# Kernel optimization log

Hardware: AMD Instinct MI355X
Metric: run time of the kernel (lower is better)

## Reference

```python
import jax, jax.numpy as jnp
import numpy as np

D_MODEL = 768
NUM_HEADS = 12
DEPTH = D_MODEL // NUM_HEADS


def setup_inputs() -> dict:
    key = jax.random.key(0)
    ks = jax.random.split(key, 11)
    B, S = 2, 2048
    scale = 1.0 / np.sqrt(D_MODEL)
    inp = {
        'v': jax.random.normal(ks[0], (B, S, D_MODEL), jnp.float32),
        'k': jax.random.normal(ks[1], (B, S, D_MODEL), jnp.float32),
        'q': jax.random.normal(ks[2], (B, S, D_MODEL), jnp.float32),
        'wq': jax.random.normal(ks[3], (D_MODEL, D_MODEL), jnp.float32) * scale,
        'bq': jnp.zeros((D_MODEL,), jnp.float32),
        'wk': jax.random.normal(ks[4], (D_MODEL, D_MODEL), jnp.float32) * scale,
        'bk': jnp.zeros((D_MODEL,), jnp.float32),
        'wv': jax.random.normal(ks[5], (D_MODEL, D_MODEL), jnp.float32) * scale,
        'bv': jnp.zeros((D_MODEL,), jnp.float32),
        'wo': jax.random.normal(ks[6], (D_MODEL, D_MODEL), jnp.float32) * scale,
        'bo': jnp.zeros((D_MODEL,), jnp.float32),
    }
    return inp


def _split_heads(x):
    B, S, _ = x.shape
    return x.reshape(B, S, NUM_HEADS, DEPTH).transpose(0, 2, 1, 3)  # [B,H,S,depth]


def reference(v, k, q, wq, bq, wk, bk, wv, bv, wo, bo):
    B, S, _ = q.shape
    qh = _split_heads(q @ wq + bq)  # [B,H,S,d]
    kh = _split_heads(k @ wk + bk)
    vh = _split_heads(v @ wv + bv)
    logits = jnp.einsum('bhqd,bhkd->bhqk', qh, kh) / jnp.sqrt(jnp.float32(DEPTH))
    attn = jax.nn.softmax(logits, axis=-1)  # [B,H,S,S]
    ctx = jnp.einsum('bhqk,bhkd->bhqd', attn, vh)
    concat = ctx.transpose(0, 2, 1, 3).reshape(B, S, D_MODEL)
    out = concat @ wo + bo
    return out, attn
```

## Files before the change

### kernel.cpp

```cpp
#include <hip/hip_runtime.h>

#define D_MODEL 768
#define NHEADS 12
#define DEPTH 64
#define SEQ 2048
#define NROWS 4096
#define KBLKS 24

typedef float f32x4 __attribute__((ext_vector_type(4)));
typedef short bf16x8 __attribute__((ext_vector_type(8)));
typedef unsigned u32x2 __attribute__((ext_vector_type(2)));
typedef unsigned u32x4 __attribute__((ext_vector_type(4)));

#define MFMA16(a, b, c) __builtin_amdgcn_mfma_f32_16x16x32_bf16((a), (b), (c), 0, 0, 0)

__device__ __forceinline__ short f2bf(float f) {
    union { float f; unsigned u; } v; v.f = f;
    unsigned r = (v.u + 0x7FFFu + ((v.u >> 16) & 1u)) >> 16;
    return (short)r;
}
__device__ __forceinline__ unsigned cvtpk(float a, float b) {
    unsigned r;
    asm("v_cvt_pk_bf16_f32 %0, %1, %2" : "=v"(r) : "v"(a), "v"(b));
    return r;
}

struct KF { bf16x8 a0, a1, b0, b1; };
struct VF { short4 x[8]; };

__device__ __forceinline__ KF loadK(const short* __restrict__ Kp, int k0, int r, int h) {
    KF f;
    const short* kr0 = Kp + (k0 + r) * DEPTH + 8 * h;
    const short* kr1 = kr0 + 16 * DEPTH;
    f.a0 = *(const bf16x8*)(kr0);
    f.a1 = *(const bf16x8*)(kr0 + 32);
    f.b0 = *(const bf16x8*)(kr1);
    f.b1 = *(const bf16x8*)(kr1 + 32);
    return f;
}
__device__ __forceinline__ VF loadV(const short* __restrict__ Vb, int k0, int r, int h) {
    VF f;
    const short* blk = Vb + (k0 >> 5) * (DEPTH * 32) + 4 * h;
#pragma unroll
    for (int nt = 0; nt < 4; nt++) {
        const short* row = blk + (16 * nt + r) * 32;
        f.x[2 * nt]     = *(const short4*)(row);
        f.x[2 * nt + 1] = *(const short4*)(row + 16);
    }
    return f;
}

__global__ __launch_bounds__(256) void xcast_kernel(
    const float* __restrict__ q, const float* __restrict__ k, const float* __restrict__ v,
    short* __restrict__ xb)
{
    int z = blockIdx.y;
    const float* src = (z == 0) ? q : (z == 1) ? k : v;
    int i = (blockIdx.x * 256 + threadIdx.x) * 8;
    int m = i / D_MODEL;
    int kk = i - m * D_MODEL;
    float4 f0 = *(const float4*)(src + i);
    float4 f1 = *(const float4*)(src + i + 4);
    u32x4 o;
    o[0] = cvtpk(f0.x, f0.y); o[1] = cvtpk(f0.z, f0.w);
    o[2] = cvtpk(f1.x, f1.y); o[3] = cvtpk(f1.z, f1.w);
    size_t off = ((size_t)(z * KBLKS + (kk >> 5)) * NROWS + m) * 32 + (kk & 31);
    *(u32x4*)(xb + off) = o;
}

__global__ __launch_bounds__(256) void wtrans_kernel(
    const float* __restrict__ wq, const float* __restrict__ wk,
    const float* __restrict__ wv, const float* __restrict__ wo,
    short* __restrict__ wt)
{
    __shared__ float tile[32][33];
    int wi = blockIdx.z;
    const float* W = (wi == 0) ? wq : (wi == 1) ? wk : (wi == 2) ? wv : wo;
    int k0 = blockIdx.x * 32, n0 = blockIdx.y * 32;
    int t = threadIdx.x;
    int tx = t & 31, ty = t >> 5;
#pragma unroll
    for (int i = 0; i < 4; i++) {
        int kk = ty + i * 8;
        tile[kk][tx] = W[(k0 + kk) * D_MODEL + n0 + tx];
    }
    __syncthreads();
    short* outb = wt + ((size_t)(wi * KBLKS + (k0 >> 5)) * D_MODEL) * 32;
#pragma unroll
    for (int i = 0; i < 4; i++) {
        int nn = ty + i * 8;
        outb[(size_t)(n0 + nn) * 32 + tx] = f2bf(tile[tx][nn]);
    }
}

__global__ __launch_bounds__(256) void qkv_gemm(
    const short* __restrict__ xb, const short* __restrict__ wt,
    const float* __restrict__ bq, const float* __restrict__ bk, const float* __restrict__ bv,
    short* __restrict__ qh, short* __restrict__ kh, short* __restrict__ vt)
{
    int z = blockIdx.z;
    int m0 = blockIdx.x * 64, n0 = blockIdx.y * 64;
    int lane = threadIdx.x & 63, w = threadIdx.x >> 6;
    int r = lane & 15, h = lane >> 4;

    const short* Ap = xb + ((size_t)z * KBLKS * NROWS + (m0 + 16 * w + r)) * 32 + 8 * h;
    const short* Bp = wt + ((size_t)z * KBLKS * D_MODEL) * 32;
    const int ASTEP = NROWS * 32, BSTEP = D_MODEL * 32;

    f32x4 acc[4] = {};
    bf16x8 ac = *(const bf16x8*)(Ap);
    bf16x8 bc[4];
#pragma unroll
    for (int nt = 0; nt < 4; nt++)
        bc[nt] = *(const bf16x8*)(Bp + (n0 + 16 * nt + r) * 32 + 8 * h);

    if (z == 2) {
        for (int kb = 0; kb < KBLKS; kb++) {
            int kn = (kb + 1 < KBLKS) ? kb + 1 : 0;
            bf16x8 an = *(const bf16x8*)(Ap + (size_t)kn * ASTEP);
            bf16x8 bn[4];
#pragma unroll
            for (int nt = 0; nt < 4; nt++)
                bn[nt] = *(const bf16x8*)(Bp + (size_t)kn * BSTEP + (n0 + 16 * nt + r) * 32 + 8 * h);
#pragma unroll
            for (int nt = 0; nt < 4; nt++)
                acc[nt] = MFMA16(ac, bc[nt], acc[nt]);
            ac = an;
#pragma unroll
            for (int nt = 0; nt < 4; nt++) bc[nt] = bn[nt];
        }
#pragma unroll
        for (int nt = 0; nt < 4; nt++) {
            int col = n0 + 16 * nt + r;
            float bsv = bv[col];
            int hh = col >> 6, dd = col & 63;
            int m = m0 + 16 * w + 4 * h;
            int b = m >> 11, s = m & 2047;
            short4 pk;
            pk.x = f2bf(acc[nt][0] + bsv);
            pk.y = f2bf(acc[nt][1] + bsv);
            pk.z = f2bf(acc[nt][2] + bsv);
            pk.w = f2bf(acc[nt][3] + bsv);
            long off = (((long)(b * NHEADS + hh) * 64 + (s >> 5)) * DEPTH + dd) * 32 + (s & 31);
            *(short4*)(vt + off) = pk;
        }
    } else {
        const float* bias = (z == 0) ? bq : bk;
        float scl = (z == 0) ? 0.18033688011112042f : 1.0f;
        short* dst = (z == 0) ? qh : kh;
        for (int kb = 0; kb < KBLKS; kb++) {
            int kn = (kb + 1 < KBLKS) ? kb + 1 : 0;
            bf16x8 an = *(const bf16x8*)(Ap + (size_t)kn * ASTEP);
            bf16x8 bn[4];
#pragma unroll
            for (int nt = 0; nt < 4; nt++)
                bn[nt] = *(const bf16x8*)(Bp + (size_t)kn * BSTEP + (n0 + 16 * nt + r) * 32 + 8 * h);
#pragma unroll
            for (int nt = 0; nt < 4; nt++)
                acc[nt] = MFMA16(bc[nt], ac, acc[nt]);
            ac = an;
#pragma unroll
            for (int nt = 0; nt < 4; nt++) bc[nt] = bn[nt];
        }
        int hh = n0 >> 6;
        int m = m0 + 16 * w + r;
        int b = m >> 11, s = m & 2047;
        long rowoff = ((long)(b * NHEADS + hh) * SEQ + s) * DEPTH;
#pragma unroll
        for (int nt = 0; nt < 4; nt++) {
            int dd = 16 * nt + 4 * h;
            float4 b4 = *(const float4*)(bias + n0 + dd);
            float v0 = (acc[nt][0] + b4.x) * scl;
            float v1 = (acc[nt][1] + b4.y) * scl;
            float v2 = (acc[nt][2] + b4.z) * scl;
            float v3 = (acc[nt][3] + b4.w) * scl;
            u32x2 pk = {cvtpk(v0, v1), cvtpk(v2, v3)};
            *(u32x2*)&dst[rowoff + dd] = pk;
        }
    }
}

__global__ __launch_bounds__(512, 4) void attn_kernel(
    const short* __restrict__ qh, const short* __restrict__ kh, const short* __restrict__ vt,
    float* __restrict__ attn, short* __restrict__ ctx)
{
    __shared__ float plds[64 * 256];
    __shared__ float sml[2][4][2][16];

    int wgid = blockIdx.x;
    int xcd = wgid & 7;
    int idx = wgid >> 3;
    int bh = xcd * 3 + (idx >> 5);
    int q0 = (idx & 31) * 64;

    int lane = threadIdx.x & 63, w = threadIdx.x >> 6;
    int wq2 = w >> 2, kc = w & 3;
    int r = lane & 15, h = lane >> 4;
    int qbase = q0 + 32 * wq2;

    const short* Qp = qh + ((long)bh * SEQ + qbase) * DEPTH;
    const short* Kp = kh + (long)bh * SEQ * DEPTH;
    const short* Vb = vt + (long)bh * (64 * DEPTH * 32);

    bf16x8 qf[2][2];
#pragma unroll
    for (int j = 0; j < 2; j++) {
        qf[j][0] = *(const bf16x8*)(Qp + (16 * j + r) * DEPTH + 8 * h);
        qf[j][1] = *(const bf16x8*)(Qp + (16 * j + r) * DEPTH + 32 + 8 * h);
    }

    float l0 = 0.f, l1 = 0.f;
    {
        int kstart = kc * 512, kend = kstart + 512;
        KF kcur = loadK(Kp, kstart, r, h);
        for (int k0 = kstart; k0 < kend; k0 += 32) {
            int kn = (k0 + 32 < kend) ? (k0 + 32) : kstart;
            KF knxt = loadK(Kp, kn, r, h);
#pragma unroll
            for (int j = 0; j < 2; j++) {
                f32x4 s0 = {}, s1 = {};
                s0 = MFMA16(kcur.a0, qf[j][0], s0);
                s1 = MFMA16(kcur.b0, qf[j][0], s1);
                s0 = MFMA16(kcur.a1, qf[j][1], s0);
                s1 = MFMA16(kcur.b1, qf[j][1], s1);
                float sum = exp2f(s0[0]) + exp2f(s0[1]) + exp2f(s0[2]) + exp2f(s0[3])
                          + exp2f(s1[0]) + exp2f(s1[1]) + exp2f(s1[2]) + exp2f(s1[3]);
                if (j == 0) l0 += sum; else l1 += sum;
            }
            kcur = knxt;
        }
    }
    l0 += __shfl_xor(l0, 16); l0 += __shfl_xor(l0, 32);
    l1 += __shfl_xor(l1, 16); l1 += __shfl_xor(l1, 32);
    if (lane < 16) {
        sml[wq2][kc][0][lane] = l0;
        sml[wq2][kc][1][lane] = l1;
    }
    __syncthreads();
    float rl[2];
#pragma unroll
    for (int j = 0; j < 2; j++)
        rl[j] = 1.0f / (sml[wq2][0][j][r] + sml[wq2][1][j][r] +
                        sml[wq2][2][j][r] + sml[wq2][3][j][r]);

    f32x4 o[2][4] = {};
    int rsw = r & 7;

    for (int chunk = 0; chunk < 8; chunk++) {
#pragma unroll
        for (int it = 0; it < 2; it++) {
            int k0 = chunk * 256 + kc * 64 + it * 32;
            KF kf = loadK(Kp, k0, r, h);
            VF vf = loadV(Vb, k0, r, h);
#pragma unroll
            for (int j = 0; j < 2; j++) {
                f32x4 s0 = {}, s1 = {};
                s0 = MFMA16(kf.a0, qf[j][0], s0);
                s1 = MFMA16(kf.b0, qf[j][0], s1);
                s0 = MFMA16(kf.a1, qf[j][1], s0);
                s1 = MFMA16(kf.b1, qf[j][1], s1);

                float p0 = exp2f(s0[0]) * rl[j], p1 = exp2f(s0[1]) * rl[j];
                float p2 = exp2f(s0[2]) * rl[j], p3 = exp2f(s0[3]) * rl[j];
                float p4 = exp2f(s1[0]) * rl[j], p5 = exp2f(s1[1]) * rl[j];
                float p6 = exp2f(s1[2]) * rl[j], p7 = exp2f(s1[3]) * rl[j];

                int row = wq2 * 32 + 16 * j + r;
                int G0 = kc * 16 + it * 8 + h;
                int G1 = G0 + 4;
                int pg0 = (G0 & ~7) | ((G0 & 7) ^ rsw);
                int pg1 = (G1 & ~7) | ((G1 & 7) ^ rsw);
                f32x4 v0 = {p0, p1, p2, p3};
                f32x4 v1 = {p4, p5, p6, p7};
                *(f32x4*)&plds[row * 256 + pg0 * 4] = v0;
                *(f32x4*)&plds[row * 256 + pg1 * 4] = v1;

                union { unsigned u[4]; bf16x8 v; } pa;
                pa.u[0] = cvtpk(p0, p1); pa.u[1] = cvtpk(p2, p3);
                pa.u[2] = cvtpk(p4, p5); pa.u[3] = cvtpk(p6, p7);
#pragma unroll
                for (int nt = 0; nt < 4; nt++) {
                    union { short4 s4[2]; bf16x8 v; } vv;
                    vv.s4[0] = vf.x[2 * nt];
                    vv.s4[1] = vf.x[2 * nt + 1];
                    o[j][nt] = MFMA16(vv.v, pa.v, o[j][nt]);
                }
            }
        }
        __syncthreads();

#pragma unroll
        for (int rr = 0; rr < 8; rr++) {
            int R = w * 8 + rr;
            float* arow = attn + ((long)(bh * SEQ + q0 + R)) * SEQ + chunk * 256;
            int pg = (lane & ~7) | ((lane & 7) ^ (R & 7));
            f32x4 val = *(const f32x4*)&plds[R * 256 + pg * 4];
            __builtin_nontemporal_store(val, (f32x4*)(arow + lane * 4));
        }
        __syncthreads();
    }

    if (kc != 0) {
#pragma unroll
        for (int j = 0; j < 2; j++)
#pragma unroll
            for (int nt = 0; nt < 4; nt++)
                *(f32x4*)&plds[((((wq2 * 3 + (kc - 1)) * 2 + j) * 4 + nt) * 64 + lane) * 4] =
                    o[j][nt];
    }
    __syncthreads();
    if (kc == 0) {
        int b = bh / NHEADS, head = bh % NHEADS;
#pragma unroll
        for (int j = 0; j < 2; j++) {
            long crow = ((long)(b * SEQ + qbase + 16 * j + r)) * D_MODEL + head * DEPTH;
#pragma unroll
            for (int nt = 0; nt < 4; nt++) {
                f32x4 acc = o[j][nt];
#pragma unroll
                for (int m = 0; m < 3; m++) {
                    f32x4 op = *(const f32x4*)
                        &plds[((((wq2 * 3 + m) * 2 + j) * 4 + nt) * 64 + lane) * 4];
                    acc[0] += op[0]; acc[1] += op[1];
                    acc[2] += op[2]; acc[3] += op[3];
                }
                *(unsigned*)&ctx[crow + 16 * nt + 4 * h]     = cvtpk(acc[0], acc[1]);
                *(unsigned*)&ctx[crow + 16 * nt + 4 * h + 2] = cvtpk(acc[2], acc[3]);
            }
        }
    }
}

__global__ __launch_bounds__(256) void out_gemm(
    const short* __restrict__ ctx, const short* __restrict__ wt,
    const float* __restrict__ bo, float* __restrict__ out)
{
    int m0 = blockIdx.x * 64, n0 = blockIdx.y * 64;
    int lane = threadIdx.x & 63, w = threadIdx.x >> 6;
    int r = lane & 15, h = lane >> 4;

    f32x4 acc[4] = {};
    const short* arow = ctx + (m0 + 16 * w + r) * D_MODEL;
    const short* Bp = wt + ((size_t)3 * KBLKS * D_MODEL) * 32;
    const int BSTEP = D_MODEL * 32;

    bf16x8 ac = *(const bf16x8*)(arow + 8 * h);
    bf16x8 bc[4];
#pragma unroll
    for (int nt = 0; nt < 4; nt++)
        bc[nt] = *(const bf16x8*)(Bp + (n0 + 16 * nt + r) * 32 + 8 * h);

    for (int kb = 0; kb < KBLKS; kb++) {
        int kn = (kb + 1 < KBLKS) ? kb + 1 : 0;
        bf16x8 an = *(const bf16x8*)(arow + kn * 32 + 8 * h);
        bf16x8 bn[4];
#pragma unroll
        for (int nt = 0; nt < 4; nt++)
            bn[nt] = *(const bf16x8*)(Bp + (size_t)kn * BSTEP + (n0 + 16 * nt + r) * 32 + 8 * h);
#pragma unroll
        for (int nt = 0; nt < 4; nt++)
            acc[nt] = MFMA16(bc[nt], ac, acc[nt]);
        ac = an;
#pragma unroll
        for (int nt = 0; nt < 4; nt++) bc[nt] = bn[nt];
    }
    int m = m0 + 16 * w + r;
#pragma unroll
    for (int nt = 0; nt < 4; nt++) {
        int n = n0 + 16 * nt + 4 * h;
        float4 b4 = *(const float4*)(bo + n);
        f32x4 res = {acc[nt][0] + b4.x, acc[nt][1] + b4.y,
                     acc[nt][2] + b4.z, acc[nt][3] + b4.w};
        *(f32x4*)(out + (long)m * D_MODEL + n) = res;
    }
}

extern "C" void kernel_launch(void* const* d_in, const int* in_sizes, int n_in,
                              void* d_out, int out_size, void* d_ws, size_t ws_size,
                              hipStream_t stream)
{
    const float* v  = (const float*)d_in[0];
    const float* k  = (const float*)d_in[1];
    const float* q  = (const float*)d_in[2];
    const float* wq = (const float*)d_in[3];
    const float* bq = (const float*)d_in[4];
    const float* wk = (const float*)d_in[5];
    const float* bk = (const float*)d_in[6];
    const float* wv = (const float*)d_in[7];
    const float* bv = (const float*)d_in[8];
    const float* wo = (const float*)d_in[9];
    const float* bo = (const float*)d_in[10];

    char* ws = (char*)d_ws;
    const size_t WT_BYTES  = (size_t)4 * D_MODEL * D_MODEL * 2;
    const size_t XB_BYTES  = (size_t)3 * NROWS * D_MODEL * 2;
    const size_t HB_BYTES  = (size_t)2 * NHEADS * SEQ * DEPTH * 2;
    short* wt  = (short*)(ws);
    short* xb  = (short*)(ws + WT_BYTES);
    short* qh  = (short*)(ws + WT_BYTES + XB_BYTES);
    short* kh  = (short*)(ws + WT_BYTES + XB_BYTES + HB_BYTES);
    short* vt  = (short*)(ws + WT_BYTES + XB_BYTES + 2 * HB_BYTES);
    short* ctx = (short*)(ws + WT_BYTES + XB_BYTES + 3 * HB_BYTES);

    float* out  = (float*)d_out;
    float* attn = (float*)d_out + (size_t)NROWS * D_MODEL;

    xcast_kernel<<<dim3(1536, 3), dim3(256), 0, stream>>>(q, k, v, xb);
    wtrans_kernel<<<dim3(24, 24, 4), dim3(256), 0, stream>>>(wq, wk, wv, wo, wt);
    qkv_gemm<<<dim3(64, 12, 3), dim3(256), 0, stream>>>(xb, wt, bq, bk, bv, qh, kh, vt);
    attn_kernel<<<dim3(768), dim3(512), 0, stream>>>(qh, kh, vt, attn, ctx);
    out_gemm<<<dim3(64, 12), dim3(256), 0, stream>>>(ctx, wt, bo, out);
}
```

Baseline: 267.5 us.

## Split softmax row-sum pass into a separate kernel writing reciprocal norms

Moves the first pass that computes softmax denominators out of attn_kernel into a new rl_kernel. It uses 384 blocks of 512 threads, each handling 128 queries with each wave covering half the key range, and writes reciprocal sums to a workspace buffer. attn_kernel then reads these values instead of recomputing them, which drops its LDS reduction and one barrier. The aim is to free attn_kernel's registers and schedule from the first pass and give the sum pass its own launch shape, at the cost of an extra launch and a small global round trip.

```diff
diff --git a/kernel.cpp b/kernel.cpp
--- a/kernel.cpp
+++ b/kernel.cpp
@@ -180,12 +180,72 @@
     }
 }
 
+__global__ __launch_bounds__(512) void rl_kernel(
+    const short* __restrict__ qh, const short* __restrict__ kh,
+    float* __restrict__ rlbuf)
+{
+    __shared__ float sml[4][2][2][16];
+
+    int wgid = blockIdx.x;
+    int xcd = wgid & 7;
+    int idx = wgid >> 3;
+    int bh = xcd * 3 + (idx >> 4);
+    int q0 = (idx & 15) * 128;
+
+    int lane = threadIdx.x & 63, w = threadIdx.x >> 6;
+    int wq2 = w >> 1, ksh = w & 1;
+    int r = lane & 15, h = lane >> 4;
+    int qbase = q0 + 32 * wq2;
+    int kstart = ksh * (SEQ / 2), kend = kstart + SEQ / 2;
+
+    const short* Qp = qh + ((long)bh * SEQ + qbase) * DEPTH;
+    const short* Kp = kh + (long)bh * SEQ * DEPTH;
+
+    bf16x8 qf[2][2];
+#pragma unroll
+    for (int j = 0; j < 2; j++) {
+        qf[j][0] = *(const bf16x8*)(Qp + (16 * j + r) * DEPTH + 8 * h);
+        qf[j][1] = *(const bf16x8*)(Qp + (16 * j + r) * DEPTH + 32 + 8 * h);
+    }
+
+    float l0 = 0.f, l1 = 0.f;
+    KF kcur = loadK(Kp, kstart, r, h);
+    for (int k0 = kstart; k0 < kend; k0 += 32) {
+        int kn = (k0 + 32 < kend) ? (k0 + 32) : kstart;
+        KF knxt = loadK(Kp, kn, r, h);
+#pragma unroll
+        for (int j = 0; j < 2; j++) {
+            f32x4 s0 = {}, s1 = {};
+            s0 = MFMA16(kcur.a0, qf[j][0], s0);
+            s1 = MFMA16(kcur.b0, qf[j][0], s1);
+            s0 = MFMA16(kcur.a1, qf[j][1], s0);
+            s1 = MFMA16(kcur.b1, qf[j][1], s1);
+            float sum = exp2f(s0[0]) + exp2f(s0[1]) + exp2f(s0[2]) + exp2f(s0[3])
+                      + exp2f(s1[0]) + exp2f(s1[1]) + exp2f(s1[2]) + exp2f(s1[3]);
+            if (j == 0) l0 += sum; else l1 += sum;
+        }
+        kcur = knxt;
+    }
+    l0 += __shfl_xor(l0, 16); l0 += __shfl_xor(l0, 32);
+    l1 += __shfl_xor(l1, 16); l1 += __shfl_xor(l1, 32);
+    if (lane < 16) {
+        sml[wq2][ksh][0][lane] = l0;
+        sml[wq2][ksh][1][lane] = l1;
+    }
+    __syncthreads();
+    if (ksh == 0 && lane < 16) {
+        float rl0 = 1.0f / (sml[wq2][0][0][lane] + sml[wq2][1][0][lane]);
+        float rl1 = 1.0f / (sml[wq2][0][1][lane] + sml[wq2][1][1][lane]);
+        rlbuf[bh * SEQ + qbase + lane]      = rl0;
+        rlbuf[bh * SEQ + qbase + 16 + lane] = rl1;
+    }
+}
+
 __global__ __launch_bounds__(512, 4) void attn_kernel(
     const short* __restrict__ qh, const short* __restrict__ kh, const short* __restrict__ vt,
-    float* __restrict__ attn, short* __restrict__ ctx)
+    const float* __restrict__ rlbuf, float* __restrict__ attn, short* __restrict__ ctx)
 {
     __shared__ float plds[64 * 256];
-    __shared__ float sml[2][4][2][16];
 
     int wgid = blockIdx.x;
     int xcd = wgid & 7;
@@ -208,40 +268,10 @@
         qf[j][0] = *(const bf16x8*)(Qp + (16 * j + r) * DEPTH + 8 * h);
         qf[j][1] = *(const bf16x8*)(Qp + (16 * j + r) * DEPTH + 32 + 8 * h);
     }
-
-    float l0 = 0.f, l1 = 0.f;
-    {
-        int kstart = kc * 512, kend = kstart + 512;
-        KF kcur = loadK(Kp, kstart, r, h);
-        for (int k0 = kstart; k0 < kend; k0 += 32) {
-            int kn = (k0 + 32 < kend) ? (k0 + 32) : kstart;
-            KF knxt = loadK(Kp, kn, r, h);
-#pragma unroll
-            for (int j = 0; j < 2; j++) {
-                f32x4 s0 = {}, s1 = {};
-                s0 = MFMA16(kcur.a0, qf[j][0], s0);
-                s1 = MFMA16(kcur.b0, qf[j][0], s1);
-                s0 = MFMA16(kcur.a1, qf[j][1], s0);
-                s1 = MFMA16(kcur.b1, qf[j][1], s1);
-                float sum = exp2f(s0[0]) + exp2f(s0[1]) + exp2f(s0[2]) + exp2f(s0[3])
-                          + exp2f(s1[0]) + exp2f(s1[1]) + exp2f(s1[2]) + exp2f(s1[3]);
-                if (j == 0) l0 += sum; else l1 += sum;
-            }
-            kcur = knxt;
-        }
-    }
-    l0 += __shfl_xor(l0, 16); l0 += __shfl_xor(l0, 32);
-    l1 += __shfl_xor(l1, 16); l1 += __shfl_xor(l1, 32);
-    if (lane < 16) {
-        sml[wq2][kc][0][lane] = l0;
-        sml[wq2][kc][1][lane] = l1;
-    }
-    __syncthreads();
     float rl[2];
 #pragma unroll
     for (int j = 0; j < 2; j++)
-        rl[j] = 1.0f / (sml[wq2][0][j][r] + sml[wq2][1][j][r] +
-                        sml[wq2][2][j][r] + sml[wq2][3][j][r]);
+        rl[j] = rlbuf[bh * SEQ + qbase + 16 * j + r];
 
     f32x4 o[2][4] = {};
     int rsw = r & 7;
@@ -395,12 +425,14 @@
     const size_t WT_BYTES  = (size_t)4 * D_MODEL * D_MODEL * 2;
     const size_t XB_BYTES  = (size_t)3 * NROWS * D_MODEL * 2;
     const size_t HB_BYTES  = (size_t)2 * NHEADS * SEQ * DEPTH * 2;
+    const size_t CTX_BYTES = (size_t)NROWS * D_MODEL * 2;
     short* wt  = (short*)(ws);
     short* xb  = (short*)(ws + WT_BYTES);
     short* qh  = (short*)(ws + WT_BYTES + XB_BYTES);
     short* kh  = (short*)(ws + WT_BYTES + XB_BYTES + HB_BYTES);
     short* vt  = (short*)(ws + WT_BYTES + XB_BYTES + 2 * HB_BYTES);
     short* ctx = (short*)(ws + WT_BYTES + XB_BYTES + 3 * HB_BYTES);
+    float* rlb = (float*)(ws + WT_BYTES + XB_BYTES + 3 * HB_BYTES + CTX_BYTES);
 
     float* out  = (float*)d_out;
     float* attn = (float*)d_out + (size_t)NROWS * D_MODEL;
@@ -408,6 +440,7 @@
     xcast_kernel<<<dim3(1536, 3), dim3(256), 0, stream>>>(q, k, v, xb);
     wtrans_kernel<<<dim3(24, 24, 4), dim3(256), 0, stream>>>(wq, wk, wv, wo, wt);
     qkv_gemm<<<dim3(64, 12, 3), dim3(256), 0, stream>>>(xb, wt, bq, bk, bv, qh, kh, vt);
-    attn_kernel<<<dim3(768), dim3(512), 0, stream>>>(qh, kh, vt, attn, ctx);
+    rl_kernel<<<dim3(384), dim3(512), 0, stream>>>(qh, kh, rlb);
+    attn_kernel<<<dim3(768), dim3(512), 0, stream>>>(qh, kh, vt, rlb, attn, ctx);
     out_gemm<<<dim3(64, 12), dim3(256), 0, stream>>>(ctx, wt, bo, out);
 }
```

Measured after the change: 288.3 us. 1.08x slower.
